# Kernel optimization log

Measured on AMD Instinct MI355X. Metric: run time of the kernel, lower is better.

## Reference

```python
import jax, jax.numpy as jnp
import numpy as np

NUM_TOPICS = 64
VOCAB_SIZE = 50000
BATCH = 2048
RHO = 0.1

def setup_inputs() -> dict:
    key = jax.random.key(0)
    k_x, k_b, k_t, k_m = jax.random.split(key, 4)
    x = jax.random.uniform(k_x, (BATCH, VOCAB_SIZE), dtype=jnp.float32)  # BoW-like counts
    beta = jax.random.normal(k_b, (NUM_TOPICS, VOCAB_SIZE), dtype=jnp.float32)
    theta = jax.random.normal(k_t, (NUM_TOPICS, NUM_TOPICS), dtype=jnp.float32)
    mu = jax.random.normal(k_m, (NUM_TOPICS,), dtype=jnp.float32)
    return {"x": x, "beta": beta, "theta": theta, "mu": mu}

def reference(x, beta, theta, mu):
    # Original double loop:
    #   log_prob[:,k] = sum(x*beta[k],1) + mu[k] + rho * sum_{j!=k} theta[k,j]*sum(x*beta[j],1)
    # Let s[b,k] = sum_v x[b,v]*beta[k,v] = (x @ beta.T)[b,k].
    # Then log_prob = s + mu + rho * s @ (theta with zeroed diagonal).T
    s = jnp.einsum('bv,kv->bk', x, beta)                      # [B, K]
    theta_off = theta * (1.0 - jnp.eye(theta.shape[0], dtype=theta.dtype))
    log_prob = s + mu[None, :] + RHO * jnp.einsum('bj,kj->bk', s, theta_off)
    return log_prob
```

## Files before the change

### kernel.cpp

```cpp
#include <hip/hip_runtime.h>

typedef unsigned short u16;
typedef unsigned int u32;
typedef unsigned long long u64;

#define VOCAB 50000
#define BATCH 2048
#define NTOP 64
#define RHO 0.1f

#define KSPLIT 16
#define CHUNK 3136
#define BM 64
#define BK 64

typedef short bf16x8 __attribute__((ext_vector_type(8)));
typedef short bf16x4 __attribute__((ext_vector_type(4)));
typedef float f32x4 __attribute__((ext_vector_type(4)));

__device__ __forceinline__ u16 f32_to_bf16(float f) {
  u32 u = __builtin_bit_cast(u32, f);
  return (u16)((u + 0x8000u) >> 16);
}
__device__ __forceinline__ u32 pack2(float a, float b) {
  return (u32)f32_to_bf16(a) | ((u32)f32_to_bf16(b) << 16);
}

__global__ void ctm_prep(const float* __restrict__ beta, u16* __restrict__ beta16,
                         float* __restrict__ s) {
  int i = blockIdx.x * blockDim.x + threadIdx.x;
  int stride = gridDim.x * blockDim.x;
  for (int j = i; j < (BATCH * NTOP / 4); j += stride)
    ((float4*)s)[j] = make_float4(0.f, 0.f, 0.f, 0.f);
  for (int j = i; j < (NTOP * VOCAB / 4); j += stride) {
    float4 v = ((const float4*)beta)[j];
    u32 lo = pack2(v.x, v.y);
    u32 hi = pack2(v.z, v.w);
    ((uint2*)beta16)[j] = make_uint2(lo, hi);
  }
}

__global__ void __launch_bounds__(256) ctm_gemm(const float* __restrict__ x,
                                                const u16* __restrict__ beta16,
                                                float* __restrict__ s) {
  __shared__ u16 ldsA[BM * BK];
  __shared__ u16 ldsB[NTOP * BK];

  const int t = threadIdx.x;
  const int l = t & 63;
  const int w = t >> 6;
  const int k0 = blockIdx.x * CHUNK;
  const int row0 = blockIdx.y * BM;
  const int kend = (k0 + CHUNK < VOCAB) ? (k0 + CHUNK) : VOCAB;
  const int nsteps = (kend - k0 + BK - 1) >> 6;

  const int arow = t >> 2;
  const int akq = (t & 3) << 4;
  const u64 xbase = (u64)(row0 + arow) * VOCAB;
  const u32 aswz = (u32)((arow & 7) << 4);
  const u32 abyte0 = (u32)(arow * 128) + (((u32)(akq * 2)) ^ aswz);
  const u32 abyte1 = (u32)(arow * 128) + (((u32)(akq * 2 + 16)) ^ aswz);

  const int bp0 = t * 16;
  const int bp1 = 4096 + t * 16;
  const int bcol0 = bp0 >> 7, bcol1 = bp1 >> 7;
  const int bk0 = ((bp0 & 127) ^ ((bcol0 & 7) << 4)) >> 1;
  const int bk1 = ((bp1 & 127) ^ ((bcol1 & 7) << 4)) >> 1;
  const u64 bsrc0 = (u64)bcol0 * VOCAB + (u64)bk0;
  const u64 bsrc1 = (u64)bcol1 * VOCAB + (u64)bk1;
  const u32 ldsb_base0 = (u32)(w * 1024) >> 1;
  const u32 ldsb_base1 = (u32)(4096 + w * 1024) >> 1;

  const int fr = l & 15;
  const int fk = l >> 4;
  const int arow_f = (w << 4) | fr;
  const u32 aswz_f = (u32)((arow_f & 7) << 4);

  f32x4 acc[4] = {{0.f,0.f,0.f,0.f},{0.f,0.f,0.f,0.f},{0.f,0.f,0.f,0.f},{0.f,0.f,0.f,0.f}};

  for (int st = 0; st < nsteps; ++st) {
    const int ks0 = k0 + (st << 6);

    __builtin_amdgcn_global_load_lds(
        (const __attribute__((address_space(1))) void*)(beta16 + bsrc0 + (u64)ks0),
        (__attribute__((address_space(3))) void*)(&ldsB[ldsb_base0]), 16, 0, 0);
    __builtin_amdgcn_global_load_lds(
        (const __attribute__((address_space(1))) void*)(beta16 + bsrc1 + (u64)ks0),
        (__attribute__((address_space(3))) void*)(&ldsB[ldsb_base1]), 16, 0, 0);

    float4 v0, v1, v2, v3;
    if (ks0 + BK <= kend) {
      const float4* xp = (const float4*)(x + xbase + ks0 + akq);
      v0 = xp[0]; v1 = xp[1]; v2 = xp[2]; v3 = xp[3];
    } else {
      float tmp[16];
      #pragma unroll
      for (int e = 0; e < 16; ++e) {
        int k = ks0 + akq + e;
        tmp[e] = (k < kend) ? x[xbase + k] : 0.0f;
      }
      v0 = make_float4(tmp[0], tmp[1], tmp[2], tmp[3]);
      v1 = make_float4(tmp[4], tmp[5], tmp[6], tmp[7]);
      v2 = make_float4(tmp[8], tmp[9], tmp[10], tmp[11]);
      v3 = make_float4(tmp[12], tmp[13], tmp[14], tmp[15]);
    }
    uint4 pk0, pk1;
    pk0.x = pack2(v0.x, v0.y); pk0.y = pack2(v0.z, v0.w);
    pk0.z = pack2(v1.x, v1.y); pk0.w = pack2(v1.z, v1.w);
    pk1.x = pack2(v2.x, v2.y); pk1.y = pack2(v2.z, v2.w);
    pk1.z = pack2(v3.x, v3.y); pk1.w = pack2(v3.z, v3.w);
    *(uint4*)(&ldsA[abyte0 >> 1]) = pk0;
    *(uint4*)(&ldsA[abyte1 >> 1]) = pk1;

    __syncthreads();

    #pragma unroll
    for (int ks = 0; ks < 2; ++ks) {
      const u32 in0 = (u32)(ks * 64 + fk * 8);
      const u32 in1 = in0 + 32;
      union { bf16x4 h[2]; bf16x8 v; } ua;
      ua.h[0] = *(const bf16x4*)(&ldsA[((u32)(arow_f * 128) + (in0 ^ aswz_f)) >> 1]);
      ua.h[1] = *(const bf16x4*)(&ldsA[((u32)(arow_f * 128) + (in1 ^ aswz_f)) >> 1]);
      #pragma unroll
      for (int n = 0; n < 4; ++n) {
        const int bcol = (n << 4) | fr;
        const u32 bswz = (u32)((bcol & 7) << 4);
        union { bf16x4 h[2]; bf16x8 v; } ub;
        ub.h[0] = *(const bf16x4*)(&ldsB[((u32)(bcol * 128) + (in0 ^ bswz)) >> 1]);
        ub.h[1] = *(const bf16x4*)(&ldsB[((u32)(bcol * 128) + (in1 ^ bswz)) >> 1]);
        acc[n] = __builtin_amdgcn_mfma_f32_16x16x32_bf16(ua.v, ub.v, acc[n], 0, 0, 0);
      }
    }
    __syncthreads();
  }

  #pragma unroll
  for (int n = 0; n < 4; ++n) {
    #pragma unroll
    for (int r = 0; r < 4; ++r) {
      const int row = row0 + (w << 4) + (fk << 2) + r;
      const int col = (n << 4) | fr;
      atomicAdd(&s[row * NTOP + col], acc[n][r]);
    }
  }
}

__global__ void __launch_bounds__(256) ctm_epi(const float* __restrict__ s,
                                               const float* __restrict__ theta,
                                               const float* __restrict__ mu,
                                               float* __restrict__ out) {
  __shared__ float thT[NTOP * NTOP];
  __shared__ float sb[8 * NTOP];
  const int t = threadIdx.x;
  const int r0 = blockIdx.x * 8;

  #pragma unroll
  for (int i = 0; i < 16; ++i) {
    int e = i * 256 + t;
    thT[(e & 63) * 64 + (e >> 6)] = theta[e];
  }
  sb[t] = s[r0 * 64 + t];
  sb[t + 256] = s[r0 * 64 + 256 + t];
  __syncthreads();

  const int k = t & 63;
  const int rl = t >> 6;
  const float muk = mu[k];
  const float diag = thT[k * 64 + k];
  #pragma unroll
  for (int rr = 0; rr < 2; ++rr) {
    const int r = rl + rr * 4;
    const float* srow = &sb[r * 64];
    float accv = 0.f;
    #pragma unroll 8
    for (int j = 0; j < 64; ++j)
      accv += thT[j * 64 + k] * srow[j];
    const float sv = srow[k];
    out[(r0 + r) * 64 + k] = sv + muk + RHO * (accv - diag * sv);
  }
}

extern "C" void kernel_launch(void* const* d_in, const int* in_sizes, int n_in,
                              void* d_out, int out_size, void* d_ws, size_t ws_size,
                              hipStream_t stream) {
  const float* x = (const float*)d_in[0];
  const float* beta = (const float*)d_in[1];
  const float* theta = (const float*)d_in[2];
  const float* mu = (const float*)d_in[3];
  float* out = (float*)d_out;

  u16* beta16 = (u16*)d_ws;
  float* s = (float*)((char*)d_ws + (size_t)NTOP * VOCAB * 2);

  ctm_prep<<<2048, 256, 0, stream>>>(beta, beta16, s);
  ctm_gemm<<<dim3(KSPLIT, BATCH / BM), 256, 0, stream>>>(x, beta16, s);
  ctm_epi<<<BATCH / 8, 256, 0, stream>>>(s, theta, mu, out);
}
```

Before: 111.4 us.

## Pre-swizzle beta into MFMA fragment layout and load GEMM operands directly to registers

The prep kernel now writes bf16 beta in a blocked layout that matches the MFMA B-fragment order, so the GEMM loads B fragments straight from global memory into registers. The x operand is also read directly into registers and converted with a packed bf16 instruction. This removes LDS staging and both block barriers per step. The K split doubles to 32 and occupancy hints are added. The cost is uncoalesced-ish per-lane x loads without LDS reuse, no software prefetch, and twice as many atomic adds into s.

```diff
diff --git a/kernel.cpp b/kernel.cpp
--- a/kernel.cpp
+++ b/kernel.cpp
@@ -9,13 +9,12 @@
 #define NTOP 64
 #define RHO 0.1f
 
-#define KSPLIT 16
-#define CHUNK 3136
-#define BM 64
-#define BK 64
+#define KSPLIT 32
+#define CHUNK 1568
+#define NKB 1563
+#define GPC 12504
 
 typedef short bf16x8 __attribute__((ext_vector_type(8)));
-typedef short bf16x4 __attribute__((ext_vector_type(4)));
 typedef float f32x4 __attribute__((ext_vector_type(4)));
 
 __device__ __forceinline__ u16 f32_to_bf16(float f) {
@@ -25,123 +24,100 @@
 __device__ __forceinline__ u32 pack2(float a, float b) {
   return (u32)f32_to_bf16(a) | ((u32)f32_to_bf16(b) << 16);
 }
+__device__ __forceinline__ u32 cvtpk(float lo, float hi) {
+  u32 r;
+  asm volatile("v_cvt_pk_bf16_f32 %0, %1, %2" : "=v"(r) : "v"(lo), "v"(hi));
+  return r;
+}
+union frag_cast { u32 w[4]; bf16x8 v; };
 
-__global__ void ctm_prep(const float* __restrict__ beta, u16* __restrict__ beta16,
+__global__ void ctm_prep(const float* __restrict__ beta, u16* __restrict__ bp,
                          float* __restrict__ s) {
   int i = blockIdx.x * blockDim.x + threadIdx.x;
   int stride = gridDim.x * blockDim.x;
   for (int j = i; j < (BATCH * NTOP / 4); j += stride)
     ((float4*)s)[j] = make_float4(0.f, 0.f, 0.f, 0.f);
-  for (int j = i; j < (NTOP * VOCAB / 4); j += stride) {
-    float4 v = ((const float4*)beta)[j];
-    u32 lo = pack2(v.x, v.y);
-    u32 hi = pack2(v.z, v.w);
-    ((uint2*)beta16)[j] = make_uint2(lo, hi);
+  for (int j = i; j < NTOP * GPC; j += stride) {
+    int col = j / GPC;
+    int g = j - col * GPC;
+    int k = g * 4;
+    float4 v = make_float4(0.f, 0.f, 0.f, 0.f);
+    if (k < VOCAB)
+      v = *(const float4*)(beta + (u64)col * VOCAB + k);
+    int kb = k >> 5;
+    int jj = k & 31;
+    int pbase = ((jj & 15) >> 2) * 8 + ((jj & 16) ? 4 : 0);
+    u32 lo = pack2(v.x, v.y), hi = pack2(v.z, v.w);
+    *(uint2*)(bp + (u64)kb * 2048 + col * 32 + pbase) = make_uint2(lo, hi);
   }
 }
 
-__global__ void __launch_bounds__(256) ctm_gemm(const float* __restrict__ x,
-                                                const u16* __restrict__ beta16,
-                                                float* __restrict__ s) {
-  __shared__ u16 ldsA[BM * BK];
-  __shared__ u16 ldsB[NTOP * BK];
-
+__global__ void __launch_bounds__(256, 4) ctm_gemm(const float* __restrict__ x,
+                                                   const u16* __restrict__ bp,
+                                                   float* __restrict__ s) {
   const int t = threadIdx.x;
   const int l = t & 63;
   const int w = t >> 6;
-  const int k0 = blockIdx.x * CHUNK;
-  const int row0 = blockIdx.y * BM;
-  const int kend = (k0 + CHUNK < VOCAB) ? (k0 + CHUNK) : VOCAB;
-  const int nsteps = (kend - k0 + BK - 1) >> 6;
-
-  const int arow = t >> 2;
-  const int akq = (t & 3) << 4;
-  const u64 xbase = (u64)(row0 + arow) * VOCAB;
-  const u32 aswz = (u32)((arow & 7) << 4);
-  const u32 abyte0 = (u32)(arow * 128) + (((u32)(akq * 2)) ^ aswz);
-  const u32 abyte1 = (u32)(arow * 128) + (((u32)(akq * 2 + 16)) ^ aswz);
-
-  const int bp0 = t * 16;
-  const int bp1 = 4096 + t * 16;
-  const int bcol0 = bp0 >> 7, bcol1 = bp1 >> 7;
-  const int bk0 = ((bp0 & 127) ^ ((bcol0 & 7) << 4)) >> 1;
-  const int bk1 = ((bp1 & 127) ^ ((bcol1 & 7) << 4)) >> 1;
-  const u64 bsrc0 = (u64)bcol0 * VOCAB + (u64)bk0;
-  const u64 bsrc1 = (u64)bcol1 * VOCAB + (u64)bk1;
-  const u32 ldsb_base0 = (u32)(w * 1024) >> 1;
-  const u32 ldsb_base1 = (u32)(4096 + w * 1024) >> 1;
-
   const int fr = l & 15;
   const int fk = l >> 4;
-  const int arow_f = (w << 4) | fr;
-  const u32 aswz_f = (u32)((arow_f & 7) << 4);
+
+  const int k0 = blockIdx.x * CHUNK;
+  const int kend = (k0 + CHUNK < VOCAB) ? (k0 + CHUNK) : VOCAB;
+  const int row = blockIdx.y * 64 + w * 16 + fr;
+
+  const float* ax = x + (u64)row * VOCAB + k0 + fk * 4;
+  const u16* bb = bp + (u64)(k0 >> 5) * 2048 + fr * 32 + fk * 8;
+
+  const int nfull = (kend - k0) >> 5;
+  const bool tail = ((kend - k0) & 31) != 0;
 
   f32x4 acc[4] = {{0.f,0.f,0.f,0.f},{0.f,0.f,0.f,0.f},{0.f,0.f,0.f,0.f},{0.f,0.f,0.f,0.f}};
 
-  for (int st = 0; st < nsteps; ++st) {
-    const int ks0 = k0 + (st << 6);
-
-    __builtin_amdgcn_global_load_lds(
-        (const __attribute__((address_space(1))) void*)(beta16 + bsrc0 + (u64)ks0),
-        (__attribute__((address_space(3))) void*)(&ldsB[ldsb_base0]), 16, 0, 0);
-    __builtin_amdgcn_global_load_lds(
-        (const __attribute__((address_space(1))) void*)(beta16 + bsrc1 + (u64)ks0),
-        (__attribute__((address_space(3))) void*)(&ldsB[ldsb_base1]), 16, 0, 0);
-
-    float4 v0, v1, v2, v3;
-    if (ks0 + BK <= kend) {
-      const float4* xp = (const float4*)(x + xbase + ks0 + akq);
-      v0 = xp[0]; v1 = xp[1]; v2 = xp[2]; v3 = xp[3];
-    } else {
-      float tmp[16];
-      #pragma unroll
-      for (int e = 0; e < 16; ++e) {
-        int k = ks0 + akq + e;
-        tmp[e] = (k < kend) ? x[xbase + k] : 0.0f;
-      }
-      v0 = make_float4(tmp[0], tmp[1], tmp[2], tmp[3]);
-      v1 = make_float4(tmp[4], tmp[5], tmp[6], tmp[7]);
-      v2 = make_float4(tmp[8], tmp[9], tmp[10], tmp[11]);
-      v3 = make_float4(tmp[12], tmp[13], tmp[14], tmp[15]);
+  #pragma unroll 2
+  for (int st = 0; st < nfull; ++st) {
+    const float4* ap = (const float4*)ax;
+    float4 a0 = ap[0];
+    float4 a1 = ap[4];
+    frag_cast ua;
+    ua.w[0] = cvtpk(a0.x, a0.y);
+    ua.w[1] = cvtpk(a0.z, a0.w);
+    ua.w[2] = cvtpk(a1.x, a1.y);
+    ua.w[3] = cvtpk(a1.z, a1.w);
+    #pragma unroll
+    for (int n = 0; n < 4; ++n) {
+      bf16x8 bf = *(const bf16x8*)(bb + n * 512);
+      acc[n] = __builtin_amdgcn_mfma_f32_16x16x32_bf16(ua.v, bf, acc[n], 0, 0, 0);
     }
-    uint4 pk0, pk1;
-    pk0.x = pack2(v0.x, v0.y); pk0.y = pack2(v0.z, v0.w);
-    pk0.z = pack2(v1.x, v1.y); pk0.w = pack2(v1.z, v1.w);
-    pk1.x = pack2(v2.x, v2.y); pk1.y = pack2(v2.z, v2.w);
-    pk1.z = pack2(v3.x, v3.y); pk1.w = pack2(v3.z, v3.w);
-    *(uint4*)(&ldsA[abyte0 >> 1]) = pk0;
-    *(uint4*)(&ldsA[abyte1 >> 1]) = pk1;
-
-    __syncthreads();
-
-    #pragma unroll
-    for (int ks = 0; ks < 2; ++ks) {
-      const u32 in0 = (u32)(ks * 64 + fk * 8);
-      const u32 in1 = in0 + 32;
-      union { bf16x4 h[2]; bf16x8 v; } ua;
-      ua.h[0] = *(const bf16x4*)(&ldsA[((u32)(arow_f * 128) + (in0 ^ aswz_f)) >> 1]);
-      ua.h[1] = *(const bf16x4*)(&ldsA[((u32)(arow_f * 128) + (in1 ^ aswz_f)) >> 1]);
-      #pragma unroll
-      for (int n = 0; n < 4; ++n) {
-        const int bcol = (n << 4) | fr;
-        const u32 bswz = (u32)((bcol & 7) << 4);
-        union { bf16x4 h[2]; bf16x8 v; } ub;
-        ub.h[0] = *(const bf16x4*)(&ldsB[((u32)(bcol * 128) + (in0 ^ bswz)) >> 1]);
-        ub.h[1] = *(const bf16x4*)(&ldsB[((u32)(bcol * 128) + (in1 ^ bswz)) >> 1]);
-        acc[n] = __builtin_amdgcn_mfma_f32_16x16x32_bf16(ua.v, ub.v, acc[n], 0, 0, 0);
-      }
-    }
-    __syncthreads();
+    ax += 32;
+    bb += 2048;
   }
 
+  if (tail) {
+    const int ks0 = k0 + (nfull << 5);
+    float av[8];
+    #pragma unroll
+    for (int e = 0; e < 8; ++e) {
+      int k = ks0 + ((e < 4) ? (fk * 4 + e) : (16 + fk * 4 + (e - 4)));
+      av[e] = (k < VOCAB) ? x[(u64)row * VOCAB + k] : 0.f;
+    }
+    frag_cast ua;
+    ua.w[0] = cvtpk(av[0], av[1]);
+    ua.w[1] = cvtpk(av[2], av[3]);
+    ua.w[2] = cvtpk(av[4], av[5]);
+    ua.w[3] = cvtpk(av[6], av[7]);
+    #pragma unroll
+    for (int n = 0; n < 4; ++n) {
+      bf16x8 bf = *(const bf16x8*)(bb + n * 512);
+      acc[n] = __builtin_amdgcn_mfma_f32_16x16x32_bf16(ua.v, bf, acc[n], 0, 0, 0);
+    }
+  }
+
+  const int orow = blockIdx.y * 64 + w * 16 + fk * 4;
   #pragma unroll
   for (int n = 0; n < 4; ++n) {
     #pragma unroll
-    for (int r = 0; r < 4; ++r) {
-      const int row = row0 + (w << 4) + (fk << 2) + r;
-      const int col = (n << 4) | fr;
-      atomicAdd(&s[row * NTOP + col], acc[n][r]);
-    }
+    for (int r = 0; r < 4; ++r)
+      atomicAdd(&s[(orow + r) * NTOP + ((n << 4) | fr)], acc[n][r]);
   }
 }
 
@@ -189,10 +165,10 @@
   const float* mu = (const float*)d_in[3];
   float* out = (float*)d_out;
 
-  u16* beta16 = (u16*)d_ws;
-  float* s = (float*)((char*)d_ws + (size_t)NTOP * VOCAB * 2);
+  u16* bp = (u16*)d_ws;
+  float* s = (float*)((char*)d_ws + 6403072u);
 
-  ctm_prep<<<2048, 256, 0, stream>>>(beta, beta16, s);
-  ctm_gemm<<<dim3(KSPLIT, BATCH / BM), 256, 0, stream>>>(x, beta16, s);
+  ctm_prep<<<2048, 256, 0, stream>>>(beta, bp, s);
+  ctm_gemm<<<dim3(KSPLIT, BATCH / 64), 256, 0, stream>>>(x, bp, s);
   ctm_epi<<<BATCH / 8, 256, 0, stream>>>(s, theta, mu, out);
 }
```

After: 130.7 us. 17.3% more time.
